# Optimization experiments

Measured on AMD Instinct MI355X. Metric: run time of the kernel, lower is better.

## Reference

```python
import jax, jax.numpy as jnp
import numpy as np

ETA = 0.01      # EMA adaptation rate
EPS = 1e-08     # numerical stability constant
BATCH, N_ASSETS = 262144, 128


def setup_inputs() -> dict:
    key = jax.random.key(0)
    k1, k2 = jax.random.split(key)
    weights = jax.random.normal(k1, (BATCH, N_ASSETS), dtype=jnp.float32)
    next_returns = jax.random.normal(k2, (BATCH, N_ASSETS), dtype=jnp.float32)
    A0 = jnp.float32(0.0)   # initial EMA of returns (module buffer A)
    B0 = jnp.float32(EPS)   # initial EMA of squared returns (module buffer B)
    return {"weights": weights, "next_returns": next_returns, "A0": A0, "B0": B0}


def reference(weights, next_returns, A0, B0):
    # portfolio return per time step: (batch,)
    R = jnp.sum(weights * next_returns, axis=1)

    def step(carry, r):
        A, Bm = carry
        dA = ETA * (r - A)
        dB = ETA * (r * r - Bm)
        var = jnp.maximum(Bm - A * A, EPS)
        D = (Bm * dA - 0.5 * A * dB) / (var ** 1.5)
        return (A + dA, Bm + dB), D

    (_, _), Ds = jax.lax.scan(step, (A0, B0), R)
    return -jnp.mean(Ds)
```

## Files before the change

### kernel.cpp

```cpp
#include <hip/hip_runtime.h>
#include <math.h>

#define BATCH     262144
#define NASSETS   128
#define TILE_ROWS 128
#define NBLK      (BATCH / TILE_ROWS)
#define SCHUNK    32
#define NSC       (BATCH / SCHUNK)
#define TBLK      64
#define TCH       (NSC / TBLK)
#define ETA       0.01
#define CDECAY    0.99
#define EPS       1e-8
#define LPAD      33

__device__ __forceinline__ float dot4(float4 a, float4 b) {
  return a.x * b.x + a.y * b.y + a.z * b.z + a.w * b.w;
}

__device__ __forceinline__ double mpow(double base, int e) {
  double r = 1.0, p = base;
  #pragma unroll
  for (int b = 0; b < 13; ++b) { if (e & (1 << b)) r *= p; p *= p; }
  return r;
}

__global__ __launch_bounds__(256) void k_rows(
    const float* __restrict__ W, const float* __restrict__ X,
    float* __restrict__ R, double* __restrict__ SA, double* __restrict__ SB) {
  __shared__ float part[TILE_ROWS * LPAD];
  const int t   = threadIdx.x;
  const int blk = blockIdx.x;
  const float4* W4 = reinterpret_cast<const float4*>(W) + (size_t)blk * 4096;
  const float4* X4 = reinterpret_cast<const float4*>(X) + (size_t)blk * 4096;

  #pragma unroll
  for (int p = 0; p < 16; ++p) {
    const int idx = p * 256 + t;
    part[(idx >> 5) * LPAD + (idx & 31)] = dot4(W4[idx], X4[idx]);
  }
  __syncthreads();

  if (t < TILE_ROWS) {
    float sum = 0.f;
    #pragma unroll
    for (int j = 0; j < 32; ++j) sum += part[t * LPAD + j];
    R[(size_t)blk * TILE_ROWS + t] = sum;

    const int e = 31 - (t & 31);
    const double c1 = CDECAY, c2 = c1*c1, c4 = c2*c2, c8 = c4*c4, c16 = c8*c8;
    double wgt = ETA;
    if (e & 1)  wgt *= c1;
    if (e & 2)  wgt *= c2;
    if (e & 4)  wgt *= c4;
    if (e & 8)  wgt *= c8;
    if (e & 16) wgt *= c16;
    const double r = (double)sum;
    double sA = wgt * r, sB = wgt * r * r;
    sA += __shfl_xor(sA, 16, 64); sB += __shfl_xor(sB, 16, 64);
    sA += __shfl_xor(sA,  8, 64); sB += __shfl_xor(sB,  8, 64);
    sA += __shfl_xor(sA,  4, 64); sB += __shfl_xor(sB,  4, 64);
    sA += __shfl_xor(sA,  2, 64); sB += __shfl_xor(sB,  2, 64);
    sA += __shfl_xor(sA,  1, 64); sB += __shfl_xor(sB,  1, 64);
    if ((t & 31) == 0) SA[blk * 4 + (t >> 5)] = sA;
    if ((t & 31) == 0) SB[blk * 4 + (t >> 5)] = sB;
  }
}

__global__ __launch_bounds__(128) void k_tail(
    const float* __restrict__ R, const double* __restrict__ SA,
    const double* __restrict__ SB, const float* __restrict__ A0p,
    const float* __restrict__ B0p, double* __restrict__ acc,
    unsigned* __restrict__ cnt, float* __restrict__ out) {
  __shared__ float  lr[TCH * LPAD];
  __shared__ double wred[4];
  const int t = threadIdx.x;
  const int b = blockIdx.x;
  const int lane = t & 63, w = t >> 6;

  const float* Rb = R + (size_t)b * (TCH * SCHUNK);
  #pragma unroll
  for (int q = 0; q < 32; ++q) {
    const int fi = q * 128 + t;
    lr[(fi >> 5) * LPAD + (fi & 31)] = Rb[fi];
  }

  double m = CDECAY;
  #pragma unroll
  for (int q = 0; q < 5; ++q) m = m * m;

  const int wbase = b * TCH - 256;
  double xA = 0.0, xB = 0.0;
  #pragma unroll
  for (int s = 0; s < 2; ++s) {
    const int j = t + s * 128;
    const int g = wbase + j;
    if (g >= 0) {
      const double wgt = mpow(m, 255 - j);
      xA += wgt * SA[g];
      xB += wgt * SB[g];
    }
  }
  #pragma unroll
  for (int d = 32; d >= 1; d >>= 1) {
    xA += __shfl_xor(xA, d, 64);
    xB += __shfl_xor(xB, d, 64);
  }
  if (lane == 0) { wred[w * 2] = xA; wred[w * 2 + 1] = xB; }
  __syncthreads();
  xA = wred[0] + wred[2];
  xB = wred[1] + wred[3];
  __syncthreads();

  const int c = b * TCH + t;
  double iA = SA[c], iB = SB[c], f = m;
  #pragma unroll
  for (int d = 1; d < 64; d <<= 1) {
    const double uA = __shfl_up(iA, d, 64);
    const double uB = __shfl_up(iB, d, 64);
    if (lane >= d) { iA += f * uA; iB += f * uB; }
    f *= f;
  }
  double eA = __shfl_up(iA, 1, 64);
  double eB = __shfl_up(iB, 1, 64);
  if (lane == 0) { eA = 0.0; eB = 0.0; }
  if (lane == 63) { wred[w * 2] = iA; wred[w * 2 + 1] = iB; }
  __syncthreads();
  const double mlane = mpow(m, lane);
  if (w == 1) { eA += wred[0] * mlane; eB += wred[1] * mlane; }

  const double mt  = mpow(m, t);
  const double hmg = mpow(m, b * TCH + t);
  double A = eA + xA * mt + (double)A0p[0] * hmg;
  double B = eB + xB * mt + (double)B0p[0] * hmg;

  double sum = 0.0;
  #pragma unroll
  for (int k = 0; k < SCHUNK; ++k) {
    const double rv = (double)lr[t * LPAD + k];
    const double dA = ETA * (rv - A);
    const double dB = ETA * (rv * rv - B);
    double var = B - A * A;
    var = var > EPS ? var : EPS;
    const double num = B * dA - 0.5 * A * dB;
    const float inv = rsqrtf((float)var);
    sum += num * (double)(inv * inv * inv);
    A += dA;
    B += dB;
  }
  #pragma unroll
  for (int d = 32; d >= 1; d >>= 1) sum += __shfl_xor(sum, d, 64);
  __syncthreads();
  if (lane == 0) wred[w] = sum;
  __syncthreads();
  if (t == 0) {
    atomicAdd(acc, wred[0] + wred[1]);
    __threadfence();
    const unsigned old = atomicAdd(cnt, 1u);
    if (old == TBLK - 1) {
      const double v = atomicAdd(acc, 0.0);
      out[0] = (float)(-v / (double)BATCH);
    }
  }
}

extern "C" void kernel_launch(void* const* d_in, const int* in_sizes, int n_in,
                              void* d_out, int out_size, void* d_ws, size_t ws_size,
                              hipStream_t stream) {
  const float* W  = (const float*)d_in[0];
  const float* X  = (const float*)d_in[1];
  const float* A0 = (const float*)d_in[2];
  const float* B0 = (const float*)d_in[3];

  char* ws = (char*)d_ws;
  float*  R  = (float*)ws;
  double* SA = (double*)(ws + (size_t)BATCH * 4);
  double* SB = SA + NSC;
  double* acc = SB + NSC;
  unsigned* cnt = (unsigned*)(acc + 1);

  hipMemsetAsync(acc, 0, 16, stream);
  k_rows<<<NBLK, 256, 0, stream>>>(W, X, R, SA, SB);
  k_tail<<<TBLK, 128, 0, stream>>>(R, SA, SB, A0, B0, acc, cnt, (float*)d_out);
}
```

Before: 56.63 us.

## Stage row tiles via direct global-to-LDS loads with halved tile size

Reduces rows per block to 64 and loads the weight and return tiles straight into shared memory with the global_load_lds builtin, then computes dot products from LDS. The per-row sum is spread across all 256 threads with a two-level reduction instead of 128 serial sums. This aims to issue more asynchronous memory traffic and better balance the reduction. In exchange it uses about 64KB of LDS per block, which can lower occupancy, and it adds extra barriers.

Result: faster. 54.78 us (-3.3%).

```diff
diff --git a/kernel.cpp b/kernel.cpp
--- a/kernel.cpp
+++ b/kernel.cpp
@@ -3,7 +3,7 @@
 
 #define BATCH     262144
 #define NASSETS   128
-#define TILE_ROWS 128
+#define TILE_ROWS 64
 #define NBLK      (BATCH / TILE_ROWS)
 #define SCHUNK    32
 #define NSC       (BATCH / SCHUNK)
@@ -28,23 +28,49 @@
 __global__ __launch_bounds__(256) void k_rows(
     const float* __restrict__ W, const float* __restrict__ X,
     float* __restrict__ R, double* __restrict__ SA, double* __restrict__ SB) {
+  __shared__ float wbuf[TILE_ROWS * NASSETS];
+  __shared__ float xbuf[TILE_ROWS * NASSETS];
   __shared__ float part[TILE_ROWS * LPAD];
+  __shared__ float hs[256];
   const int t   = threadIdx.x;
   const int blk = blockIdx.x;
-  const float4* W4 = reinterpret_cast<const float4*>(W) + (size_t)blk * 4096;
-  const float4* X4 = reinterpret_cast<const float4*>(X) + (size_t)blk * 4096;
-
-  #pragma unroll
-  for (int p = 0; p < 16; ++p) {
+  const int w   = t >> 6, l = t & 63;
+  const float4* W4 = reinterpret_cast<const float4*>(W) + (size_t)blk * 1024;
+  const float4* X4 = reinterpret_cast<const float4*>(X) + (size_t)blk * 1024;
+
+  #pragma unroll
+  for (int j = 0; j < 8; ++j) {
+    const int seg = w * 8 + j;
+    const float4* gw = W4 + seg * 64 + l;
+    const float4* gx = X4 + seg * 64 + l;
+    __builtin_amdgcn_global_load_lds(
+        (const __attribute__((address_space(1))) void*)gw,
+        (__attribute__((address_space(3))) void*)&wbuf[seg * 256], 16, 0, 0);
+    __builtin_amdgcn_global_load_lds(
+        (const __attribute__((address_space(1))) void*)gx,
+        (__attribute__((address_space(3))) void*)&xbuf[seg * 256], 16, 0, 0);
+  }
+  __syncthreads();
+
+  #pragma unroll
+  for (int p = 0; p < 8; ++p) {
     const int idx = p * 256 + t;
-    part[(idx >> 5) * LPAD + (idx & 31)] = dot4(W4[idx], X4[idx]);
-  }
-  __syncthreads();
-
+    const float4 a = reinterpret_cast<const float4*>(wbuf)[idx];
+    const float4 b = reinterpret_cast<const float4*>(xbuf)[idx];
+    part[(idx >> 5) * LPAD + (idx & 31)] = dot4(a, b);
+  }
+  __syncthreads();
+
+  {
+    const int row = t & 63, q = t >> 6;
+    float s = 0.f;
+    #pragma unroll
+    for (int j = 0; j < 8; ++j) s += part[row * LPAD + q * 8 + j];
+    hs[t] = s;
+  }
+  __syncthreads();
   if (t < TILE_ROWS) {
-    float sum = 0.f;
-    #pragma unroll
-    for (int j = 0; j < 32; ++j) sum += part[t * LPAD + j];
+    const float sum = hs[t] + hs[t + 64] + hs[t + 128] + hs[t + 192];
     R[(size_t)blk * TILE_ROWS + t] = sum;
 
     const int e = 31 - (t & 31);
@@ -62,8 +88,10 @@
     sA += __shfl_xor(sA,  4, 64); sB += __shfl_xor(sB,  4, 64);
     sA += __shfl_xor(sA,  2, 64); sB += __shfl_xor(sB,  2, 64);
     sA += __shfl_xor(sA,  1, 64); sB += __shfl_xor(sB,  1, 64);
-    if ((t & 31) == 0) SA[blk * 4 + (t >> 5)] = sA;
-    if ((t & 31) == 0) SB[blk * 4 + (t >> 5)] = sB;
+    if ((t & 31) == 0) {
+      SA[blk * 2 + (t >> 5)] = sA;
+      SB[blk * 2 + (t >> 5)] = sB;
+    }
   }
 }
 
```
